# Kernel optimization log

Hardware: AMD Instinct MI355X
Metric: run time of the kernel (lower is better)

## Reference

```python
import jax, jax.numpy as jnp
import numpy as np

N_EMBD = 1024
N_HEAD = 16
HEAD_SIZE = N_EMBD // N_HEAD
EPS = 1e-5


def layernorm(x, g, b):
    mu = jnp.mean(x, axis=-1, keepdims=True)
    var = jnp.var(x, axis=-1, keepdims=True)
    return (x - mu) * jax.lax.rsqrt(var + EPS) * g + b


def setup_inputs() -> dict:
    key = jax.random.key(0)
    ks = jax.random.split(key, 12)
    s = 0.02
    C = N_EMBD
    return {
        "x": jax.random.normal(ks[0], (2, 2048, C), dtype=jnp.float32),
        "Wq": jax.random.normal(ks[1], (C, C), dtype=jnp.float32) * s,
        "Wk": jax.random.normal(ks[2], (C, C), dtype=jnp.float32) * s,
        "Wv": jax.random.normal(ks[3], (C, C), dtype=jnp.float32) * s,
        "Wo": jax.random.normal(ks[4], (C, C), dtype=jnp.float32) * s,
        "bo": jnp.zeros((C,), dtype=jnp.float32),
        "W1": jax.random.normal(ks[5], (C, 4 * C), dtype=jnp.float32) * s,
        "b1": jnp.zeros((4 * C,), dtype=jnp.float32),
        "W2": jax.random.normal(ks[6], (4 * C, C), dtype=jnp.float32) * s,
        "b2": jnp.zeros((C,), dtype=jnp.float32),
        "ln1_g": jnp.ones((C,), dtype=jnp.float32),
        "ln1_b": jnp.zeros((C,), dtype=jnp.float32),
        "ln2_g": jnp.ones((C,), dtype=jnp.float32),
        "ln2_b": jnp.zeros((C,), dtype=jnp.float32),
    }


def reference(x, Wq, Wk, Wv, Wo, bo, W1, b1, W2, b2, ln1_g, ln1_b, ln2_g, ln2_b):
    B, T, C = x.shape
    H, Dh = N_HEAD, HEAD_SIZE

    # --- self-attention branch ---
    h = layernorm(x, ln1_g, ln1_b)
    q = (h @ Wq).reshape(B, T, H, Dh)
    k = (h @ Wk).reshape(B, T, H, Dh)
    v = (h @ Wv).reshape(B, T, H, Dh)

    # NOTE: original scales by C**-0.5 (n_embd), not head_size**-0.5
    scale = C ** (-0.5)
    scores = jnp.einsum("bqhd,bkhd->bhqk", q, k) * scale  # [B,H,T,T]
    causal = jnp.tril(jnp.ones((T, T), dtype=bool))
    scores = jnp.where(causal, scores, -jnp.inf)
    wei = jax.nn.softmax(scores, axis=-1)
    attn = jnp.einsum("bhqk,bkhd->bqhd", wei, v).reshape(B, T, C)
    x = x + attn @ Wo + bo

    # --- MLP branch ---
    h2 = layernorm(x, ln2_g, ln2_b)
    ff = jax.nn.relu(h2 @ W1 + b1) @ W2 + b2
    return x + ff
```

## Files before the change

### kernel.cpp

```cpp
#include <hip/hip_runtime.h>

typedef unsigned short u16;
typedef __bf16 bf16;
typedef bf16 bf16x8 __attribute__((ext_vector_type(8)));
typedef float f32x4 __attribute__((ext_vector_type(4)));


__device__ __forceinline__ u16 f2bf(float f) {
  bf16 b = (bf16)f;
  return __builtin_bit_cast(u16, b);
}

__device__ __forceinline__ void gll16(void* lds, const void* g) {
  __builtin_amdgcn_global_load_lds((__attribute__((address_space(1))) void*)g,
                                   (__attribute__((address_space(3))) void*)lds,
                                   16, 0, 0);
}

__device__ __forceinline__ f32x4 mfma16(bf16x8 a, bf16x8 b, f32x4 c) {
  return __builtin_amdgcn_mfma_f32_16x16x32_bf16(a, b, c, 0, 0, 0);
}


__global__ __launch_bounds__(256)
void transpose_all(const float* __restrict__ Wq, const float* __restrict__ Wk,
                   const float* __restrict__ Wv, const float* __restrict__ Wo,
                   const float* __restrict__ W1, const float* __restrict__ W2,
                   u16* __restrict__ WqT, u16* __restrict__ WkT,
                   u16* __restrict__ WvT, u16* __restrict__ WoT,
                   u16* __restrict__ W1T, u16* __restrict__ W2T) {
  __shared__ float tile[32][33];
  const int id = blockIdx.x;
  const float* src;
  u16* dst;
  int R, C, t;
  if (id < 4096) {
    const int w = id >> 10;
    t = id & 1023; R = 1024; C = 1024;
    src = w == 0 ? Wq : w == 1 ? Wk : w == 2 ? Wv : Wo;
    dst = w == 0 ? WqT : w == 1 ? WkT : w == 2 ? WvT : WoT;
  } else if (id < 8192) {
    t = id - 4096; R = 1024; C = 4096; src = W1; dst = W1T;
  } else {
    t = id - 8192; R = 4096; C = 1024; src = W2; dst = W2T;
  }
  const int tilesx = C >> 5;
  const int c0 = (t % tilesx) * 32, r0 = (t / tilesx) * 32;
  const int tx = threadIdx.x, ty = threadIdx.y;
#pragma unroll
  for (int i = 0; i < 4; ++i)
    tile[ty + i * 8][tx] = src[(size_t)(r0 + ty + i * 8) * C + c0 + tx];
  __syncthreads();
#pragma unroll
  for (int i = 0; i < 4; ++i)
    dst[(size_t)(c0 + ty + i * 8) * R + r0 + tx] = f2bf(tile[tx][ty + i * 8]);
}


__global__ __launch_bounds__(256)
void ln_kernel(const float* __restrict__ x, const float* __restrict__ g,
               const float* __restrict__ bb, u16* __restrict__ h) {
  const int row = blockIdx.x;
  const int tid = threadIdx.x;
  const float4 xv = ((const float4*)(x + (size_t)row * 1024))[tid];
  float s = xv.x + xv.y + xv.z + xv.w;
  float q = xv.x * xv.x + xv.y * xv.y + xv.z * xv.z + xv.w * xv.w;
#pragma unroll
  for (int m = 1; m < 64; m <<= 1) {
    s += __shfl_xor(s, m);
    q += __shfl_xor(q, m);
  }
  __shared__ float ss[4], qq[4];
  const int wid = tid >> 6, lane = tid & 63;
  if (lane == 0) { ss[wid] = s; qq[wid] = q; }
  __syncthreads();
  s = ss[0] + ss[1] + ss[2] + ss[3];
  q = qq[0] + qq[1] + qq[2] + qq[3];
  const float mean = s * (1.0f / 1024.0f);
  const float var = q * (1.0f / 1024.0f) - mean * mean;
  const float rs = rsqrtf(var + 1e-5f);
  const float4 gv = ((const float4*)g)[tid];
  const float4 bv = ((const float4*)bb)[tid];
  ushort4 o;
  o.x = f2bf((xv.x - mean) * rs * gv.x + bv.x);
  o.y = f2bf((xv.y - mean) * rs * gv.y + bv.y);
  o.z = f2bf((xv.z - mean) * rs * gv.z + bv.z);
  o.w = f2bf((xv.w - mean) * rs * gv.w + bv.w);
  ((ushort4*)(h + (size_t)row * 1024))[tid] = o;
}


__device__ __forceinline__ void xcd_swizzle(int& bx, int& by, int& bz) {
  const int gx = gridDim.x, gy = gridDim.y;
  const int nwg = gx * gy * (int)gridDim.z;
  int flat = (int)blockIdx.x + gx * ((int)blockIdx.y + gy * (int)blockIdx.z);
  flat = (flat & 7) * (nwg >> 3) + (flat >> 3);
  bx = flat % gx;
  const int rem = flat / gx;
  by = rem % gy;
  bz = rem / gy;
}


template <int EPI>
__global__ __launch_bounds__(256)
void gemm_bt(const u16* __restrict__ A, const u16* __restrict__ Bt,
             const float* __restrict__ bias,
             void* __restrict__ O0, void* __restrict__ O1, void* __restrict__ O2,
             int M, int N, int K) {
  __shared__ __align__(16) u16 Alds[3][128 * 32];
  __shared__ __align__(16) u16 Blds[3][128 * 32];
  const int tid = threadIdx.x;
  const int lane = tid & 63, wid = tid >> 6;
  const int rl = lane & 15, kg = lane >> 4;
  const int ksw = (rl >> 1) & 3;
  int bx, by, bz;
  xcd_swizzle(bx, by, bz);
  const int m0 = by * 128, n0 = bx * 128;
  f32x4 acc[4][4];
#pragma unroll
  for (int i = 0; i < 4; ++i)
#pragma unroll
    for (int j = 0; j < 4; ++j) acc[i][j] = (f32x4){0.f, 0.f, 0.f, 0.f};
  const int wr = wid >> 1, wc = wid & 1;
  const int c0 = wid * 2, c1 = wid * 2 + 1;
  const int srow0 = c0 * 16 + (lane >> 2);
  const int srow1 = c1 * 16 + (lane >> 2);
  const int skol = (((lane & 3) ^ ((lane >> 3) & 3))) * 8;

#define STAGE_BT(buf, k0)                                                      \
  {                                                                            \
    gll16(Alds[buf] + c0 * 512, A + (size_t)(m0 + srow0) * K + (k0) + skol);   \
    gll16(Alds[buf] + c1 * 512, A + (size_t)(m0 + srow1) * K + (k0) + skol);   \
    gll16(Blds[buf] + c0 * 512, Bt + (size_t)(n0 + srow0) * K + (k0) + skol);  \
    gll16(Blds[buf] + c1 * 512, Bt + (size_t)(n0 + srow1) * K + (k0) + skol);  \
  }

  const int nt = K >> 5;
  STAGE_BT(0, 0);
  STAGE_BT(1, 32);
  int cur = 0;
  for (int t = 0; t < nt; ++t) {
    if (t + 1 < nt)
      asm volatile("s_waitcnt vmcnt(4)" ::: "memory");
    else
      asm volatile("s_waitcnt vmcnt(0)" ::: "memory");
    __builtin_amdgcn_s_barrier();
    if (t + 2 < nt) {
      const int nxt = cur >= 1 ? cur - 1 : cur + 2;
      STAGE_BT(nxt, (t + 2) << 5);
    }
    bf16x8 af[4], bfr[4];
#pragma unroll
    for (int m = 0; m < 4; ++m)
      af[m] = *(const bf16x8*)(Alds[cur] + (wr * 64 + m * 16 + rl) * 32 +
                               (kg ^ ksw) * 8);
#pragma unroll
    for (int n = 0; n < 4; ++n)
      bfr[n] = *(const bf16x8*)(Blds[cur] + (wc * 64 + n * 16 + rl) * 32 +
                                (kg ^ ksw) * 8);
    __builtin_amdgcn_s_setprio(1);
#pragma unroll
    for (int m = 0; m < 4; ++m)
#pragma unroll
      for (int n = 0; n < 4; ++n)
        acc[m][n] = mfma16(af[m], bfr[n], acc[m][n]);
    __builtin_amdgcn_s_setprio(0);
    cur = cur + 1 == 3 ? 0 : cur + 1;
  }
#undef STAGE_BT

#pragma unroll
  for (int m = 0; m < 4; ++m) {
#pragma unroll
    for (int n = 0; n < 4; ++n) {
      const int col = n0 + wc * 64 + n * 16 + rl;
      const int row0 = m0 + wr * 64 + m * 16 + kg * 4;
      if (EPI == 0) {
        const int seg = col >> 10;
        const int lc = col & 1023;
        if (seg == 2) {
          u16* vt = (u16*)O2;
          const size_t off =
              ((size_t)((row0 >> 11) * 16 + (lc >> 6)) * 64 + (lc & 63)) * 2048 +
              (row0 & 2047);
          ushort4 pk = {f2bf(acc[m][n][0]), f2bf(acc[m][n][1]),
                        f2bf(acc[m][n][2]), f2bf(acc[m][n][3])};
          *(ushort4*)(vt + off) = pk;
        } else {
          u16* o = (u16*)(seg == 0 ? O0 : O1);
#pragma unroll
          for (int r = 0; r < 4; ++r)
            o[(size_t)(row0 + r) * 1024 + lc] = f2bf(acc[m][n][r]);
        }
      } else {
        const float bv = bias[col];
#pragma unroll
        for (int r = 0; r < 4; ++r) {
          float v = acc[m][n][r] + bv;
          v = v > 0.f ? v : 0.f;
          ((u16*)O0)[(size_t)(row0 + r) * N + col] = f2bf(v);
        }
      }
    }
  }
}


__global__ __launch_bounds__(256)
void gemm64(const u16* __restrict__ A, const u16* __restrict__ Bt,
            const float* __restrict__ bias, const float* __restrict__ res,
            float* __restrict__ O, int M, int N, int K) {
  __shared__ __align__(16) u16 Alds[3][64 * 64];
  __shared__ __align__(16) u16 Blds[3][128 * 64];
  const int tid = threadIdx.x;
  const int lane = tid & 63, wid = tid >> 6;
  const int rl = lane & 15, kg = lane >> 4;
  int bx, by, bz;
  xcd_swizzle(bx, by, bz);
  const int m0 = by * 64, n0 = bx * 128;
  f32x4 acc[2][4];
#pragma unroll
  for (int i = 0; i < 2; ++i)
#pragma unroll
    for (int j = 0; j < 4; ++j) acc[i][j] = (f32x4){0.f, 0.f, 0.f, 0.f};
  const int wr = wid >> 1, wc = wid & 1;
  const int lrow = lane >> 3;
  const int lslot = lane & 7;

#define SRCA(base_r, k0)                                                       \
  (A + (size_t)(m0 + (base_r) + lrow) * K + (k0) +                             \
   ((lslot ^ (((base_r) + lrow) & 7)) * 8))
#define SRCB(base_r, k0)                                                       \
  (Bt + (size_t)(n0 + (base_r) + lrow) * K + (k0) +                            \
   ((lslot ^ (((base_r) + lrow) & 7)) * 8))

#define STAGE_64(buf, k0)                                                      \
  {                                                                            \
    gll16(Alds[buf] + (wid * 16 + 0) * 64, SRCA(wid * 16 + 0, k0));            \
    gll16(Alds[buf] + (wid * 16 + 8) * 64, SRCA(wid * 16 + 8, k0));            \
    gll16(Blds[buf] + (wid * 32 + 0) * 64, SRCB(wid * 32 + 0, k0));            \
    gll16(Blds[buf] + (wid * 32 + 8) * 64, SRCB(wid * 32 + 8, k0));            \
    gll16(Blds[buf] + (wid * 32 + 16) * 64, SRCB(wid * 32 + 16, k0));          \
    gll16(Blds[buf] + (wid * 32 + 24) * 64, SRCB(wid * 32 + 24, k0));          \
  }

  const int nt = K >> 6;
  STAGE_64(0, 0);
  STAGE_64(1, 64);
  int cur = 0;
  for (int t = 0; t < nt; ++t) {
    if (t + 1 < nt)
      asm volatile("s_waitcnt vmcnt(6)" ::: "memory");
    else
      asm volatile("s_waitcnt vmcnt(0)" ::: "memory");
    __builtin_amdgcn_s_barrier();
    if (t + 2 < nt) {
      const int nxt = cur >= 1 ? cur - 1 : cur + 2;
      STAGE_64(nxt, (t + 2) << 6);
    }
    bf16x8 af[2][2], bfr[4][2];
#pragma unroll
    for (int m = 0; m < 2; ++m) {
      const int row = wr * 32 + m * 16 + rl;
#pragma unroll
      for (int kf = 0; kf < 2; ++kf)
        af[m][kf] = *(const bf16x8*)(Alds[cur] + row * 64 +
                                     ((kf * 4 + kg) ^ (row & 7)) * 8);
    }
#pragma unroll
    for (int n = 0; n < 4; ++n) {
      const int row = wc * 64 + n * 16 + rl;
#pragma unroll
      for (int kf = 0; kf < 2; ++kf)
        bfr[n][kf] = *(const bf16x8*)(Blds[cur] + row * 64 +
                                      ((kf * 4 + kg) ^ (row & 7)) * 8);
    }
    __builtin_amdgcn_s_setprio(1);
#pragma unroll
    for (int m = 0; m < 2; ++m)
#pragma unroll
      for (int n = 0; n < 4; ++n) {
        acc[m][n] = mfma16(af[m][0], bfr[n][0], acc[m][n]);
        acc[m][n] = mfma16(af[m][1], bfr[n][1], acc[m][n]);
      }
    __builtin_amdgcn_s_setprio(0);
    cur = cur + 1 == 3 ? 0 : cur + 1;
  }
#undef STAGE_64
#undef SRCA
#undef SRCB

#pragma unroll
  for (int m = 0; m < 2; ++m) {
#pragma unroll
    for (int n = 0; n < 4; ++n) {
      const int col = n0 + wc * 64 + n * 16 + rl;
      const int row0 = m0 + wr * 32 + m * 16 + kg * 4;
      const float bv = bias[col];
#pragma unroll
      for (int r = 0; r < 4; ++r) {
        const int row = row0 + r;
        O[(size_t)row * N + col] =
            acc[m][n][r] + bv + res[(size_t)row * N + col];
      }
    }
  }
}


#define SC2 0.045084220027780106f

__device__ __forceinline__ void attn_range(
    const u16* __restrict__ qg, const u16* __restrict__ kgl,
    const u16* __restrict__ vtb, size_t rowb, int cb, char* plw,
    int rl, int kg, int q0, int kvb, int kve, bool mask_last,
    f32x4 (&ot)[2][4], float (&lrun)[2]) {
  if (kvb >= kve) return;
  const int swz = (rl & 7) << 4;
  bf16x8 qf[2][2];
#pragma unroll
  for (int m = 0; m < 2; ++m) {
    const u16* qp = qg + (rowb + q0 + m * 16 + rl) * 1024 + cb + kg * 8;
    qf[m][0] = *(const bf16x8*)(qp);
    qf[m][1] = *(const bf16x8*)(qp + 32);
  }

  bf16x8 ka[4][2], kb[4][2];
#define LOADK(dst, kvi)                                                        \
  {                                                                            \
    const u16* krow = kgl + (rowb + (kvi) * 64 + rl) * 1024 + cb + kg * 8;     \
    _Pragma("unroll") for (int n = 0; n < 4; ++n) {                            \
      dst[n][0] = *(const bf16x8*)(krow + (size_t)n * 16 * 1024);              \
      dst[n][1] = *(const bf16x8*)(krow + (size_t)n * 16 * 1024 + 32);         \
    }                                                                          \
  }

#define BODY(kf, kvi)                                                          \
  {                                                                            \
    const int kv0 = (kvi) * 64;                                                \
    const u16* vrow = vtb + (size_t)rl * 2048 + kv0 + kg * 8;                  \
    bf16x8 vfr[4][2];                                                          \
    _Pragma("unroll") for (int dt = 0; dt < 4; ++dt) {                         \
      vfr[dt][0] = *(const bf16x8*)(vrow + (size_t)dt * 16 * 2048);            \
      vfr[dt][1] = *(const bf16x8*)(vrow + (size_t)dt * 16 * 2048 + 32);       \
    }                                                                          \
    const bool domask = mask_last && ((kvi) == kve - 1);                       \
    _Pragma("unroll") for (int m = 0; m < 2; ++m) {                            \
      f32x4 s[4];                                                              \
      __builtin_amdgcn_s_setprio(1);                                           \
      _Pragma("unroll") for (int n = 0; n < 4; ++n) {                          \
        f32x4 t = (f32x4){0.f, 0.f, 0.f, 0.f};                                 \
        t = mfma16(kf[n][0], qf[m][0], t);                                     \
        t = mfma16(kf[n][1], qf[m][1], t);                                     \
        s[n] = t;                                                              \
      }                                                                        \
      __builtin_amdgcn_s_setprio(0);                                           \
      if (domask) {                                                            \
        const int qrow = q0 + m * 16 + rl;                                     \
        _Pragma("unroll") for (int n = 0; n < 4; ++n)                          \
            _Pragma("unroll") for (int r = 0; r < 4; ++r) {                    \
          const int tk = kv0 + n * 16 + 4 * kg + r;                            \
          s[n][r] = (tk > qrow) ? -3e38f : s[n][r];                            \
        }                                                                      \
      }                                                                        \
      float ps = 0.f;                                                          \
      _Pragma("unroll") for (int n = 0; n < 4; ++n) {                          \
        const float p0 = exp2f(__builtin_fmaf(s[n][0], SC2, -8.f));            \
        const float p1 = exp2f(__builtin_fmaf(s[n][1], SC2, -8.f));            \
        const float p2 = exp2f(__builtin_fmaf(s[n][2], SC2, -8.f));            \
        const float p3 = exp2f(__builtin_fmaf(s[n][3], SC2, -8.f));            \
        ps += (p0 + p1) + (p2 + p3);                                           \
        ushort4 pk = {f2bf(p0), f2bf(p1), f2bf(p2), f2bf(p3)};                 \
        *(ushort4*)(plw + m * 2048 + ((rl * 128 + n * 32 + kg * 8) ^ swz)) =   \
            pk;                                                                \
      }                                                                        \
      lrun[m] += ps;                                                           \
    }                                                                          \
    _Pragma("unroll") for (int m = 0; m < 2; ++m) {                            \
      const bf16x8 pf0 =                                                       \
          *(const bf16x8*)(plw + m * 2048 + ((rl * 128 + kg * 16) ^ swz));     \
      const bf16x8 pf1 = *(const bf16x8*)(plw + m * 2048 +                     \
                                          ((rl * 128 + 64 + kg * 16) ^ swz));  \
      __builtin_amdgcn_s_setprio(1);                                           \
      _Pragma("unroll") for (int dt = 0; dt < 4; ++dt) {                       \
        ot[m][dt] = mfma16(vfr[dt][0], pf0, ot[m][dt]);                        \
        ot[m][dt] = mfma16(vfr[dt][1], pf1, ot[m][dt]);                        \
      }                                                                        \
      __builtin_amdgcn_s_setprio(0);                                           \
    }                                                                          \
  }

  LOADK(ka, kvb);
  int kv = kvb;
  for (;;) {
    if (kv + 1 < kve) LOADK(kb, kv + 1);
    BODY(ka, kv);
    ++kv;
    if (kv >= kve) break;
    if (kv + 1 < kve) LOADK(ka, kv + 1);
    BODY(kb, kv);
    ++kv;
    if (kv >= kve) break;
  }
#undef LOADK
#undef BODY
}

__global__ __launch_bounds__(256)
void attn_kernel(const u16* __restrict__ qg, const u16* __restrict__ kgl,
                 const u16* __restrict__ vtg, u16* __restrict__ og) {
  const int tid = threadIdx.x, lane = tid & 63, wid = tid >> 6;
  const int rl = lane & 15, kg = lane >> 4;
  const int flat = blockIdx.x;
  const int bh = (flat & 7) * 4 + ((flat >> 3) & 3);
  const int j = 63 - (flat >> 5);
  const int q0 = j * 32;
  const int nkv = (j >> 1) + 1;
  const int kb = (nkv * wid) >> 2;
  const int ke = (nkv * (wid + 1)) >> 2;
  const size_t rowb = (size_t)(bh >> 4) * 2048;
  const int cb = (bh & 15) * 64;
  const u16* vtb = vtg + (size_t)bh * 64 * 2048;

  __shared__ __align__(16) char Pl[4][4096];
  __shared__ __align__(16) f32x4 PartO[4][2][4][64];
  __shared__ float PartL[4][2][16];

  f32x4 ot[2][4];
  float lrun[2] = {0.f, 0.f};
#pragma unroll
  for (int m = 0; m < 2; ++m)
#pragma unroll
    for (int dt = 0; dt < 4; ++dt) ot[m][dt] = (f32x4){0.f, 0.f, 0.f, 0.f};

  attn_range(qg, kgl, vtb, rowb, cb, Pl[wid], rl, kg, q0, kb, ke,
             wid == 3, ot, lrun);

#pragma unroll
  for (int m = 0; m < 2; ++m) {
    lrun[m] += __shfl_xor(lrun[m], 16);
    lrun[m] += __shfl_xor(lrun[m], 32);
#pragma unroll
    for (int dt = 0; dt < 4; ++dt) PartO[wid][m][dt][lane] = ot[m][dt];
    if (kg == 0) PartL[wid][m][rl] = lrun[m];
  }
  __syncthreads();

  if (wid < 2) {
    const int m = wid;
    const float l = PartL[0][m][rl] + PartL[1][m][rl] +
                    PartL[2][m][rl] + PartL[3][m][rl];
    const float inv = 1.f / l;
    u16* orow = og + (rowb + q0 + m * 16 + rl) * 1024 + cb;
#pragma unroll
    for (int dt = 0; dt < 4; ++dt) {
      const f32x4 o = PartO[0][m][dt][lane] + PartO[1][m][dt][lane] +
                      PartO[2][m][dt][lane] + PartO[3][m][dt][lane];
      ushort4 ok = {f2bf(o[0] * inv), f2bf(o[1] * inv),
                    f2bf(o[2] * inv), f2bf(o[3] * inv)};
      *(ushort4*)(orow + dt * 16 + 4 * kg) = ok;
    }
  }
}


extern "C" void kernel_launch(void* const* d_in, const int* in_sizes, int n_in,
                              void* d_out, int out_size, void* d_ws, size_t ws_size,
                              hipStream_t stream) {
  const float* x    = (const float*)d_in[0];
  const float* Wq   = (const float*)d_in[1];
  const float* Wk   = (const float*)d_in[2];
  const float* Wv   = (const float*)d_in[3];
  const float* Wo   = (const float*)d_in[4];
  const float* bo   = (const float*)d_in[5];
  const float* W1   = (const float*)d_in[6];
  const float* b1   = (const float*)d_in[7];
  const float* W2   = (const float*)d_in[8];
  const float* b2   = (const float*)d_in[9];
  const float* ln1g = (const float*)d_in[10];
  const float* ln1b = (const float*)d_in[11];
  const float* ln2g = (const float*)d_in[12];
  const float* ln2b = (const float*)d_in[13];
  float* out = (float*)d_out;

  char* ws = (char*)d_ws;
  const size_t MB = 1024 * 1024;
  u16* WqT  = (u16*)(ws + 0 * MB);
  u16* WoT  = (u16*)(ws + 6 * MB);
  u16* W1T  = (u16*)(ws + 8 * MB);
  u16* W2T  = (u16*)(ws + 16 * MB);
  u16* h    = (u16*)(ws + 24 * MB);
  u16* q    = (u16*)(ws + 32 * MB);
  u16* k    = (u16*)(ws + 40 * MB);
  u16* vt   = (u16*)(ws + 48 * MB);
  u16* attn = (u16*)(ws + 56 * MB);
  float* x1 = (float*)(ws + 64 * MB);
  u16* ff1  = (u16*)(ws + 32 * MB);
  u16* WkT  = WqT + 1024 * 1024;
  u16* WvT  = WqT + 2 * 1024 * 1024;

  dim3 tblk(32, 8);
  transpose_all<<<12288, tblk, 0, stream>>>(Wq, Wk, Wv, Wo, W1, W2,
                                            WqT, WkT, WvT, WoT, W1T, W2T);

  ln_kernel<<<4096, 256, 0, stream>>>(x, ln1g, ln1b, h);

  gemm_bt<0><<<dim3(24, 32), 256, 0, stream>>>(h, WqT, nullptr,
                                               q, k, vt, 4096, 3072, 1024);

  attn_kernel<<<2048, 256, 0, stream>>>(q, k, vt, attn);

  gemm64<<<dim3(8, 64), 256, 0, stream>>>(attn, WoT, bo, x, x1,
                                          4096, 1024, 1024);

  ln_kernel<<<4096, 256, 0, stream>>>(x1, ln2g, ln2b, h);

  gemm_bt<1><<<dim3(32, 32), 256, 0, stream>>>(h, W1T, b1, ff1, ff1, ff1,
                                               4096, 4096, 1024);

  gemm64<<<dim3(8, 64), 256, 0, stream>>>(ff1, W2T, b2, x1, out,
                                          4096, 1024, 4096);
}
```

Measured before the change: 273.0 us.

## Pair light and heavy causal query tiles per two-wave attention block

The attention kernel now runs 1024 blocks of two waves instead of 2048 blocks of four waves. Each block handles a pair of query tiles, a light early one and a heavy late one, so causal work is balanced. Wave 0 finishes the light tile and part of the heavy tile, wave 1 does the rest of the heavy tile, and the two partial results are merged through LDS. This cuts the cross-wave reduction and LDS footprint, at the cost of fewer waves per block and less latency hiding within a block.

```diff
diff --git a/kernel.cpp b/kernel.cpp
--- a/kernel.cpp
+++ b/kernel.cpp
@@ -407,25 +407,25 @@
 #undef BODY
 }
 
-__global__ __launch_bounds__(256)
+__global__ __launch_bounds__(128)
 void attn_kernel(const u16* __restrict__ qg, const u16* __restrict__ kgl,
                  const u16* __restrict__ vtg, u16* __restrict__ og) {
   const int tid = threadIdx.x, lane = tid & 63, wid = tid >> 6;
   const int rl = lane & 15, kg = lane >> 4;
   const int flat = blockIdx.x;
   const int bh = (flat & 7) * 4 + ((flat >> 3) & 3);
-  const int j = 63 - (flat >> 5);
-  const int q0 = j * 32;
-  const int nkv = (j >> 1) + 1;
-  const int kb = (nkv * wid) >> 2;
-  const int ke = (nkv * (wid + 1)) >> 2;
+  const int pr = flat >> 5;
+  const int jA = pr, jB = 63 - pr;
+  const int nA = (jA >> 1) + 1, nB = (jB >> 1) + 1;
+  const int a = (nB - nA) >> 1;
   const size_t rowb = (size_t)(bh >> 4) * 2048;
   const int cb = (bh & 15) * 64;
   const u16* vtb = vtg + (size_t)bh * 64 * 2048;
 
-  __shared__ __align__(16) char Pl[4][4096];
-  __shared__ __align__(16) f32x4 PartO[4][2][4][64];
-  __shared__ float PartL[4][2][16];
+  __shared__ __align__(16) char Pl[2][4096];
+  __shared__ __align__(16) float MrgO[2][4][64][4];
+  __shared__ float MrgL[2][16];
+  char* plw = Pl[wid];
 
   f32x4 ot[2][4];
   float lrun[2] = {0.f, 0.f};
@@ -434,32 +434,57 @@
 #pragma unroll
     for (int dt = 0; dt < 4; ++dt) ot[m][dt] = (f32x4){0.f, 0.f, 0.f, 0.f};
 
-  attn_range(qg, kgl, vtb, rowb, cb, Pl[wid], rl, kg, q0, kb, ke,
-             wid == 3, ot, lrun);
-
-#pragma unroll
-  for (int m = 0; m < 2; ++m) {
-    lrun[m] += __shfl_xor(lrun[m], 16);
-    lrun[m] += __shfl_xor(lrun[m], 32);
-#pragma unroll
-    for (int dt = 0; dt < 4; ++dt) PartO[wid][m][dt][lane] = ot[m][dt];
-    if (kg == 0) PartL[wid][m][rl] = lrun[m];
+  if (wid == 0) {
+    attn_range(qg, kgl, vtb, rowb, cb, plw, rl, kg, jA * 32, 0, nA, true,
+               ot, lrun);
+#pragma unroll
+    for (int m = 0; m < 2; ++m) {
+      lrun[m] += __shfl_xor(lrun[m], 16);
+      lrun[m] += __shfl_xor(lrun[m], 32);
+      const float inv = 1.f / lrun[m];
+      u16* orow = og + (rowb + jA * 32 + m * 16 + rl) * 1024 + cb;
+#pragma unroll
+      for (int dt = 0; dt < 4; ++dt) {
+        ushort4 ok = {f2bf(ot[m][dt][0] * inv), f2bf(ot[m][dt][1] * inv),
+                      f2bf(ot[m][dt][2] * inv), f2bf(ot[m][dt][3] * inv)};
+        *(ushort4*)(orow + dt * 16 + 4 * kg) = ok;
+      }
+      lrun[m] = 0.f;
+#pragma unroll
+      for (int dt = 0; dt < 4; ++dt) ot[m][dt] = (f32x4){0.f, 0.f, 0.f, 0.f};
+    }
+    attn_range(qg, kgl, vtb, rowb, cb, plw, rl, kg, jB * 32, 0, a, false,
+               ot, lrun);
+  } else {
+    attn_range(qg, kgl, vtb, rowb, cb, plw, rl, kg, jB * 32, a, nB, true,
+               ot, lrun);
+#pragma unroll
+    for (int m = 0; m < 2; ++m) {
+      lrun[m] += __shfl_xor(lrun[m], 16);
+      lrun[m] += __shfl_xor(lrun[m], 32);
+#pragma unroll
+      for (int dt = 0; dt < 4; ++dt)
+        *(f32x4*)(&MrgO[m][dt][lane][0]) = ot[m][dt];
+      if (kg == 0) MrgL[m][rl] = lrun[m];
+    }
   }
   __syncthreads();
-
-  if (wid < 2) {
-    const int m = wid;
-    const float l = PartL[0][m][rl] + PartL[1][m][rl] +
-                    PartL[2][m][rl] + PartL[3][m][rl];
-    const float inv = 1.f / l;
-    u16* orow = og + (rowb + q0 + m * 16 + rl) * 1024 + cb;
-#pragma unroll
-    for (int dt = 0; dt < 4; ++dt) {
-      const f32x4 o = PartO[0][m][dt][lane] + PartO[1][m][dt][lane] +
-                      PartO[2][m][dt][lane] + PartO[3][m][dt][lane];
-      ushort4 ok = {f2bf(o[0] * inv), f2bf(o[1] * inv),
-                    f2bf(o[2] * inv), f2bf(o[3] * inv)};
-      *(ushort4*)(orow + dt * 16 + 4 * kg) = ok;
+  if (wid == 0) {
+#pragma unroll
+    for (int m = 0; m < 2; ++m) {
+      lrun[m] += __shfl_xor(lrun[m], 16);
+      lrun[m] += __shfl_xor(lrun[m], 32);
+      const float inv = 1.f / (lrun[m] + MrgL[m][rl]);
+      u16* orow = og + (rowb + jB * 32 + m * 16 + rl) * 1024 + cb;
+#pragma unroll
+      for (int dt = 0; dt < 4; ++dt) {
+        const f32x4 o1 = *(const f32x4*)(&MrgO[m][dt][lane][0]);
+        ushort4 ok;
+#pragma unroll
+        for (int r = 0; r < 4; ++r)
+          ((u16*)&ok)[r] = f2bf((ot[m][dt][r] + o1[r]) * inv);
+        *(ushort4*)(orow + dt * 16 + 4 * kg) = ok;
+      }
     }
   }
 }
@@ -509,7 +534,7 @@
   gemm_bt<0><<<dim3(24, 32), 256, 0, stream>>>(h, WqT, nullptr,
                                                q, k, vt, 4096, 3072, 1024);
 
-  attn_kernel<<<2048, 256, 0, stream>>>(q, k, vt, attn);
+  attn_kernel<<<1024, 128, 0, stream>>>(q, k, vt, attn);
 
   gemm64<<<dim3(8, 64), 256, 0, stream>>>(attn, WoT, bo, x, x1,
                                           4096, 1024, 1024);
```

Result: faster. 254.9 us (-6.6%).
